# Performance work log

Measured on AMD Instinct MI355X. Metric: run time of the kernel, lower is better.

The kernel has to match this reference:

```python
import jax, jax.numpy as jnp
import numpy as np

N = 74240        # total nodes (256 graphs x 290 padded atoms)
E = 593920       # edges
D_IN = 75        # atom feature dim (dgllife canonical featurizer)
D = 128          # embedding / hidden dim
L = 3            # GCN layers
BATCH = 256      # graphs per batch
EPS = 1e-5


def setup_inputs() -> dict:
    key = jax.random.key(0)
    ks = jax.random.split(key, 10)
    node_feats = jax.random.normal(ks[0], (N, D_IN), dtype=jnp.float32)
    src = jax.random.randint(ks[1], (E,), 0, N, dtype=jnp.int32)
    dst = jax.random.randint(ks[2], (E,), 0, N, dtype=jnp.int32)
    # init linear, bias=False; padding=True zeros the last OUTPUT unit's weights
    W_init = jax.random.normal(ks[3], (D_IN, D), dtype=jnp.float32) * 0.05
    W_init = W_init.at[:, -1].set(0.0)
    # per-layer params (stacked): GraphConv weight/bias, residual Linear, BatchNorm
    Wg = jax.random.normal(ks[4], (L, D, D), dtype=jnp.float32) * 0.05
    bg = jnp.zeros((L, D), dtype=jnp.float32)
    Wr = jax.random.normal(ks[5], (L, D, D), dtype=jnp.float32) * 0.05
    br = jnp.zeros((L, D), dtype=jnp.float32)
    gamma = jnp.ones((L, D), dtype=jnp.float32)
    beta = jnp.zeros((L, D), dtype=jnp.float32)
    return {"node_feats": node_feats, "src": src, "dst": dst, "W_init": W_init,
            "Wg": Wg, "bg": bg, "Wr": Wr, "br": br, "gamma": gamma, "beta": beta}


def reference(node_feats, src, dst, W_init, Wg, bg, Wr, br, gamma, beta):
    # initial node embedding (no bias)
    h = node_feats @ W_init                                   # [N, D]
    for l in range(L):
        # GraphConv, gnn_norm='none': sum over in-neighbors, then linear + relu
        agg = jax.ops.segment_sum(h[src], dst, num_segments=N)   # [N, D] irregular gather/scatter
        gc = jax.nn.relu(agg @ Wg[l] + bg[l])
        # residual branch: Linear + same activation
        res = jax.nn.relu(h @ Wr[l] + br[l])
        h2 = gc + res
        # BatchNorm1d over nodes (training-mode batch statistics, dropout=0)
        mu = jnp.mean(h2, axis=0)
        var = jnp.var(h2, axis=0)
        h = gamma[l] * (h2 - mu) * jax.lax.rsqrt(var + EPS) + beta[l]
    return h.reshape(BATCH, -1, D)                            # [256, 290, 128]
```

## Files before the change

### kernel.cpp

```cpp
#include <hip/hip_runtime.h>

#define NN 74240
#define NE 593920
#define DIN 75
#define DD 128
#define NL 3
#define EPS 1e-5f
#define NB 290
#define NT (NN / 64)
#define NREP 64
#define SROWX 104

#define NB_WIFRAG 48
#define NZ4 ((NL * NREP * 256 + NN) / 4)
#define NB_ZERO  ((NZ4 + 255) / 256)
#define NB_PRE   (NB_WIFRAG + NB_ZERO)

#define NB_INIT  (NN / 64)
#define SB_WPREP NB_INIT
#define NB_WPREP ((NL * 2 * 16384) / 256)
#define SB_HIST  (SB_WPREP + NB_WPREP)
#define NB_HIST  (NE / 256)
#define SB_PREP  (SB_HIST + NB_HIST)
#define NB_SETUP (SB_PREP + 1)

typedef __attribute__((ext_vector_type(8))) short short8;
typedef __attribute__((ext_vector_type(4))) float f32x4;

static __device__ __forceinline__ unsigned short f2bf(float f) {
    union { float f; unsigned u; } v; v.f = f;
    unsigned u = v.u;
    unsigned r = (u + 0x7fffu + ((u >> 16) & 1u)) >> 16;
    return (unsigned short)r;
}

static __device__ __forceinline__ float bf2f(unsigned short s) {
    union { unsigned u; float f; } v; v.u = ((unsigned)s) << 16; return v.f;
}

__global__ __launch_bounds__(256) void k_pre(const float* __restrict__ Wi,
                                             unsigned short* __restrict__ wifrag,
                                             int* __restrict__ zbase) {
    const int tid = threadIdx.x;
    const int b = blockIdx.x;
    if (b < NB_WIFRAG) {
        const int e = b * 256 + tid;
        const int j = e & 7;
        const int lane = (e >> 3) & 63;
        const int st = e >> 9;
        const int s = st >> 3, t = st & 7;
        const int k = s * 32 + (lane >> 4) * 8 + j;
        const int n = t * 16 + (lane & 15);
        wifrag[e] = (k < DIN) ? f2bf(Wi[k * DD + n]) : (unsigned short)0;
    } else {
        const int zi = (b - NB_WIFRAG) * 256 + tid;
        if (zi < NZ4) {
            ((int4*)zbase)[zi] = (int4){0, 0, 0, 0};
        }
    }
}

__global__ __launch_bounds__(256) void k_setup(const float* __restrict__ X,
                                               const unsigned short* __restrict__ wifrag,
                                               unsigned short* __restrict__ hb,
                                               const float* __restrict__ Wg,
                                               const float* __restrict__ Wr,
                                               unsigned short* __restrict__ wf,
                                               const int* __restrict__ dst,
                                               int* __restrict__ cnt,
                                               float* __restrict__ ab0) {
    __shared__ unsigned short sXb[64 * SROWX];
    const int tid = threadIdx.x;
    const int b = blockIdx.x;
    if (b < NB_INIT) {
        const int r0 = b * 64;
        {
            const int row = tid >> 2;
            const int qt = tid & 3;
            const int k0 = qt * 19;
            const int k1 = (qt == 3) ? DIN : k0 + 19;
            const float* xrow = X + (size_t)(r0 + row) * DIN;
            unsigned short* srow = sXb + row * SROWX;
            for (int k = k0; k < k1; ++k) srow[k] = f2bf(xrow[k]);
            if (qt == 3) {
                for (int k = DIN; k < SROWX; ++k) srow[k] = 0;
            }
        }
        __syncthreads();
        const int w = tid >> 6;
        const int lane = tid & 63;
        const int ln15 = lane & 15;
        const int q = lane >> 4;
        const short8* __restrict__ wif = (const short8*)wifrag;
        f32x4 acc[8];
        #pragma unroll
        for (int t = 0; t < 8; ++t) acc[t] = (f32x4){0.f, 0.f, 0.f, 0.f};
        #pragma unroll
        for (int s = 0; s < 3; ++s) {
            const int ks = s * 32 + q * 8;
            const short8 af = *(const short8*)&sXb[(w * 16 + ln15) * SROWX + ks];
            #pragma unroll
            for (int t = 0; t < 8; ++t) {
                const short8 bfr = wif[(s * 8 + t) * 64 + lane];
                acc[t] = __builtin_amdgcn_mfma_f32_16x16x32_bf16(af, bfr, acc[t], 0, 0, 0);
            }
        }
        #pragma unroll
        for (int t = 0; t < 8; ++t) {
            #pragma unroll
            for (int r = 0; r < 4; ++r) {
                hb[(size_t)(r0 + w * 16 + q * 4 + r) * DD + t * 16 + ln15] = f2bf(acc[t][r]);
            }
        }
    } else if (b < SB_HIST) {
        const int gt = (b - SB_WPREP) * 256 + tid;
        const int l = gt >> 15;
        const int m = (gt >> 14) & 1;
        const int e = gt & 16383;
        const int k = e >> 7, n = e & 127;
        const float* W = (m == 0 ? Wg : Wr) + l * 16384;
        const float v = W[e];
        const int s = k >> 5, q = (k >> 3) & 3, j = k & 7, t = n >> 4;
        const int ln = (q << 4) | (n & 15);
        const int idx = ((s * 8 + t) * 64 + ln) * 8 + j;
        wf[(l * 2 + m) * 16384 + idx] = f2bf(v);
    } else if (b < SB_PREP) {
        const int e = (b - SB_HIST) * 256 + tid;
        atomicAdd(&cnt[dst[e]], 1);
    } else {
        ab0[tid] = (tid < 128) ? 1.0f : 0.0f;
    }
}

__global__ __launch_bounds__(256) void k_scan1(const int* __restrict__ cnt,
                                               int* __restrict__ bsum) {
    const int tid = threadIdx.x;
    int v = cnt[blockIdx.x * 256 + tid];
    #pragma unroll
    for (int off = 1; off < 64; off <<= 1) v += __shfl_xor(v, off, 64);
    __shared__ int ws[4];
    if ((tid & 63) == 0) ws[tid >> 6] = v;
    __syncthreads();
    if (tid == 0) bsum[blockIdx.x] = ws[0] + ws[1] + ws[2] + ws[3];
}

__global__ __launch_bounds__(256) void k_scan3(const int* __restrict__ cnt,
                                               const int* __restrict__ bsum,
                                               int* __restrict__ rowptr,
                                               int* __restrict__ offs) {
    const int tid = threadIdx.x;
    const int b = blockIdx.x;
    const int t = b * 256 + tid;
    const int lane = tid & 63;
    __shared__ int ws[4];
    __shared__ int ws2[4];
    __shared__ int sBoff;
    int part = 0;
    for (int i = tid; i < b; i += 256) part += bsum[i];
    #pragma unroll
    for (int off = 1; off < 64; off <<= 1) part += __shfl_xor(part, off, 64);
    if (lane == 0) ws2[tid >> 6] = part;
    __syncthreads();
    if (tid == 0) sBoff = ws2[0] + ws2[1] + ws2[2] + ws2[3];
    const int v = cnt[t];
    int inc = v;
    #pragma unroll
    for (int off = 1; off < 64; off <<= 1) {
        const int u = __shfl_up(inc, off, 64);
        if (lane >= off) inc += u;
    }
    if (lane == 63) ws[tid >> 6] = inc;
    __syncthreads();
    const int w = tid >> 6;
    int waveoff = 0;
    for (int i = 0; i < 4; ++i) waveoff += (i < w) ? ws[i] : 0;
    const int excl = sBoff + waveoff + inc - v;
    rowptr[t] = excl;
    offs[t] = excl;
    if (b == NB - 1 && tid == 255) rowptr[NN] = NE;
}

__global__ __launch_bounds__(256) void k_fill(const int* __restrict__ src,
                                              const int* __restrict__ dst,
                                              int* offs, int* __restrict__ col) {
    const int e = blockIdx.x * 256 + threadIdx.x;
    const int pos = atomicAdd(&offs[dst[e]], 1);
    col[pos] = src[e];
}

__global__ __launch_bounds__(128) void k_stats(const float* __restrict__ srep,
                                               const float* __restrict__ gamma,
                                               const float* __restrict__ beta,
                                               float* __restrict__ ab) {
    const int c = threadIdx.x;
    float s = 0.f, q = 0.f;
    for (int r = 0; r < NREP; ++r) {
        s += srep[r * 256 + c];
        q += srep[r * 256 + 128 + c];
    }
    const float invN = 1.0f / (float)NN;
    const float mu = s * invN;
    const float var = q * invN - mu * mu;
    const float a = gamma[c] * rsqrtf(var + EPS);
    ab[c] = a;
    ab[128 + c] = beta[c] - a * mu;
}

__global__ __launch_bounds__(256) void k_gather(const unsigned short* __restrict__ hb,
                                                const int* __restrict__ rowptr,
                                                const int* __restrict__ col,
                                                const float* __restrict__ ab,
                                                unsigned short* __restrict__ aggb) {
    const int wave = threadIdx.x >> 6;
    const int lane = threadIdx.x & 63;
    const int row = blockIdx.x * 4 + wave;
    const int eb = rowptr[row];
    const int ee = rowptr[row + 1];
    const int half = lane >> 5;
    const int f = (lane & 31) * 4;
    float4 a0 = {0.f,0.f,0.f,0.f}, a1 = {0.f,0.f,0.f,0.f};
    float4 a2 = {0.f,0.f,0.f,0.f}, a3 = {0.f,0.f,0.f,0.f};
    int e = eb + half;
    for (; e + 6 < ee; e += 8) {
        const int c0 = col[e], c1 = col[e + 2], c2 = col[e + 4], c3 = col[e + 6];
        const ushort4 v0 = *(const ushort4*)(hb + (size_t)c0 * DD + f);
        const ushort4 v1 = *(const ushort4*)(hb + (size_t)c1 * DD + f);
        const ushort4 v2 = *(const ushort4*)(hb + (size_t)c2 * DD + f);
        const ushort4 v3 = *(const ushort4*)(hb + (size_t)c3 * DD + f);
        a0.x += bf2f(v0.x); a0.y += bf2f(v0.y); a0.z += bf2f(v0.z); a0.w += bf2f(v0.w);
        a1.x += bf2f(v1.x); a1.y += bf2f(v1.y); a1.z += bf2f(v1.z); a1.w += bf2f(v1.w);
        a2.x += bf2f(v2.x); a2.y += bf2f(v2.y); a2.z += bf2f(v2.z); a2.w += bf2f(v2.w);
        a3.x += bf2f(v3.x); a3.y += bf2f(v3.y); a3.z += bf2f(v3.z); a3.w += bf2f(v3.w);
    }
    for (; e < ee; e += 2) {
        const int c = col[e];
        const ushort4 v = *(const ushort4*)(hb + (size_t)c * DD + f);
        a0.x += bf2f(v.x); a0.y += bf2f(v.y); a0.z += bf2f(v.z); a0.w += bf2f(v.w);
    }
    float4 s;
    s.x = (a0.x + a1.x) + (a2.x + a3.x);
    s.y = (a0.y + a1.y) + (a2.y + a3.y);
    s.z = (a0.z + a1.z) + (a2.z + a3.z);
    s.w = (a0.w + a1.w) + (a2.w + a3.w);
    s.x += __shfl_xor(s.x, 32, 64);
    s.y += __shfl_xor(s.y, 32, 64);
    s.z += __shfl_xor(s.z, 32, 64);
    s.w += __shfl_xor(s.w, 32, 64);
    if (half == 0) {
        const float deg = (float)(ee - eb);
        const float4 av = *(const float4*)(ab + f);
        const float4 bv = *(const float4*)(ab + 128 + f);
        ushort4 o;
        o.x = f2bf(fmaf(av.x, s.x, deg * bv.x));
        o.y = f2bf(fmaf(av.y, s.y, deg * bv.y));
        o.z = f2bf(fmaf(av.z, s.z, deg * bv.z));
        o.w = f2bf(fmaf(av.w, s.w, deg * bv.w));
        *(ushort4*)(aggb + (size_t)row * DD + f) = o;
    }
}

#define STAGE(bf, ss) do {                                              \
    _Pragma("unroll")                                                   \
    for (int i_ = 0; i_ < 4; ++i_) {                                    \
        const int idx_ = tid + i_ * 256;                                \
        const uint4 v_ = (idx_ < 512) ? wg_u4[(ss) * 512 + idx_]        \
                                      : wr_u4[(ss) * 512 + idx_ - 512]; \
        ((uint4*)sB[bf])[idx_] = v_;                                    \
    }                                                                   \
} while (0)

__global__ __launch_bounds__(256, 4) void k_layer(const unsigned short* __restrict__ hin,
                                                  const unsigned short* __restrict__ aggb,
                                                  const unsigned short* __restrict__ wfrag,
                                                  const float* __restrict__ bg,
                                                  const float* __restrict__ br,
                                                  const float* __restrict__ ab,
                                                  unsigned short* __restrict__ h2b,
                                                  float* __restrict__ sumrep) {
    __shared__ unsigned short sB[2][8192];
    __shared__ float sSum[256];
    const int tid = threadIdx.x;
    sSum[tid] = 0.0f;

    const int w = tid >> 6;
    const int lane = tid & 63;
    const int ln15 = lane & 15;
    const int q = lane >> 4;
    const int r0 = blockIdx.x * 64 + w * 16;
    const int arow = r0 + ln15;

    const uint4* __restrict__ wg_u4 = (const uint4*)wfrag;
    const uint4* __restrict__ wr_u4 = wg_u4 + 2048;

    f32x4 accg[8], accr[8];
    #pragma unroll
    for (int t = 0; t < 8; ++t) {
        accg[t] = (f32x4){0.f, 0.f, 0.f, 0.f};
        accr[t] = (f32x4){0.f, 0.f, 0.f, 0.f};
    }

    STAGE(0, 0);
    __syncthreads();
    int cur = 0;

    #pragma unroll
    for (int s = 0; s < 4; ++s) {
        if (s < 3) STAGE(cur ^ 1, s + 1);
        const int kk = s * 32 + q * 8;
        const short8 af = *(const short8*)(aggb + (size_t)arow * DD + kk);
        const short8 hr = *(const short8*)(hin + (size_t)arow * DD + kk);
        const float4 av0 = *(const float4*)(ab + kk);
        const float4 av1 = *(const float4*)(ab + kk + 4);
        const float4 bv0 = *(const float4*)(ab + 128 + kk);
        const float4 bv1 = *(const float4*)(ab + 128 + kk + 4);
        short8 hf;
        hf[0] = (short)f2bf(fmaf(av0.x, bf2f((unsigned short)hr[0]), bv0.x));
        hf[1] = (short)f2bf(fmaf(av0.y, bf2f((unsigned short)hr[1]), bv0.y));
        hf[2] = (short)f2bf(fmaf(av0.z, bf2f((unsigned short)hr[2]), bv0.z));
        hf[3] = (short)f2bf(fmaf(av0.w, bf2f((unsigned short)hr[3]), bv0.w));
        hf[4] = (short)f2bf(fmaf(av1.x, bf2f((unsigned short)hr[4]), bv1.x));
        hf[5] = (short)f2bf(fmaf(av1.y, bf2f((unsigned short)hr[5]), bv1.y));
        hf[6] = (short)f2bf(fmaf(av1.z, bf2f((unsigned short)hr[6]), bv1.z));
        hf[7] = (short)f2bf(fmaf(av1.w, bf2f((unsigned short)hr[7]), bv1.w));
        #pragma unroll
        for (int t = 0; t < 8; ++t) {
            const short8 bgf = *(const short8*)&sB[cur][(t * 64 + lane) * 8];
            const short8 brf = *(const short8*)&sB[cur][4096 + (t * 64 + lane) * 8];
            accg[t] = __builtin_amdgcn_mfma_f32_16x16x32_bf16(af, bgf, accg[t], 0, 0, 0);
            accr[t] = __builtin_amdgcn_mfma_f32_16x16x32_bf16(hf, brf, accr[t], 0, 0, 0);
        }
        __syncthreads();
        cur ^= 1;
    }

    #pragma unroll
    for (int t = 0; t < 8; ++t) {
        const int c = t * 16 + ln15;
        const float bgc = bg[c];
        const float brc = br[c];
        float sv = 0.f, qv = 0.f;
        #pragma unroll
        for (int r = 0; r < 4; ++r) {
            const int row = r0 + q * 4 + r;
            const float v = fmaxf(accg[t][r] + bgc, 0.f) + fmaxf(accr[t][r] + brc, 0.f);
            h2b[(size_t)row * DD + c] = f2bf(v);
            sv += v; qv += v * v;
        }
        sv += __shfl_xor(sv, 16, 64); sv += __shfl_xor(sv, 32, 64);
        qv += __shfl_xor(qv, 16, 64); qv += __shfl_xor(qv, 32, 64);
        if (q == 0) {
            atomicAdd(&sSum[c], sv);
            atomicAdd(&sSum[128 + c], qv);
        }
    }
    __syncthreads();
    atomicAdd(&sumrep[(blockIdx.x & (NREP - 1)) * 256 + tid], sSum[tid]);
}

__global__ __launch_bounds__(256) void k_bn(const unsigned short* __restrict__ h2b,
                                            const float* __restrict__ ab,
                                            float* __restrict__ out) {
    const int t = blockIdx.x * 256 + threadIdx.x;
    const size_t base = (size_t)t * 4;
    const int c = (int)(base & 127);
    const ushort4 v = *(const ushort4*)(h2b + base);
    const float4 a = *(const float4*)(ab + c);
    const float4 b = *(const float4*)(ab + 128 + c);
    float4 o;
    o.x = fmaf(a.x, bf2f(v.x), b.x);
    o.y = fmaf(a.y, bf2f(v.y), b.y);
    o.z = fmaf(a.z, bf2f(v.z), b.z);
    o.w = fmaf(a.w, bf2f(v.w), b.w);
    *(float4*)(out + base) = o;
}

extern "C" void kernel_launch(void* const* d_in, const int* in_sizes, int n_in,
                              void* d_out, int out_size, void* d_ws, size_t ws_size,
                              hipStream_t stream) {
    const float* X     = (const float*)d_in[0];
    const int*   src   = (const int*)d_in[1];
    const int*   dst   = (const int*)d_in[2];
    const float* Wi    = (const float*)d_in[3];
    const float* Wg    = (const float*)d_in[4];
    const float* bg    = (const float*)d_in[5];
    const float* Wr    = (const float*)d_in[6];
    const float* br    = (const float*)d_in[7];
    const float* gamma = (const float*)d_in[8];
    const float* beta  = (const float*)d_in[9];
    float* out = (float*)d_out;

    unsigned short* hA   = (unsigned short*)d_ws;
    unsigned short* hB   = hA + (size_t)NN * DD;
    unsigned short* aggb = hB + (size_t)NN * DD;
    float* sumrep = (float*)(aggb + (size_t)NN * DD);
    int* cnt      = (int*)(sumrep + NL * NREP * 256);
    int* offs     = cnt + NN;
    float* abv    = (float*)(offs + NN);
    unsigned short* wfrag = (unsigned short*)(abv + (NL + 1) * 2 * DD);
    unsigned short* wifrag = wfrag + NL * 2 * 16384;
    int* rowptr = (int*)(wifrag + 12288);
    int* col    = rowptr + NN + 1;
    int* bsum   = col + NE;

    k_pre<<<NB_PRE, 256, 0, stream>>>(Wi, wifrag, (int*)sumrep);
    k_setup<<<NB_SETUP, 256, 0, stream>>>(X, wifrag, hA, Wg, Wr, wfrag, dst, cnt, abv);
    k_scan1<<<NB, 256, 0, stream>>>(cnt, bsum);
    k_scan3<<<NB, 256, 0, stream>>>(cnt, bsum, rowptr, offs);
    k_fill<<<NE / 256, 256, 0, stream>>>(src, dst, offs, col);

    const unsigned short* hcur = hA;
    unsigned short* h2bufs[NL] = { hB, hA, hB };
    for (int l = 0; l < NL; ++l) {
        const float* abl = abv + l * 2 * DD;
        unsigned short* h2 = h2bufs[l];
        k_gather<<<NN / 4, 256, 0, stream>>>(hcur, rowptr, col, abl, aggb);
        k_layer<<<NT, 256, 0, stream>>>(hcur, aggb,
                                        wfrag + l * 2 * 16384,
                                        bg + l * DD, br + l * DD,
                                        abl, h2, sumrep + (size_t)l * NREP * 256);
        k_stats<<<1, 128, 0, stream>>>(sumrep + (size_t)l * NREP * 256, gamma + l * DD,
                                       beta + l * DD, abv + (l + 1) * 2 * DD);
        if (l == NL - 1) {
            k_bn<<<(NN * 32) / 256, 256, 0, stream>>>(h2, abv + NL * 2 * DD, out);
        }
        hcur = h2;
    }
}
```

Baseline: 279.4 us.

## Fold BN stats into gather launch, move affine to layer, vectorize X load

Moves the per-layer BatchNorm statistics reduction into an extra block of the next gather kernel, removing two k_stats launches. The gather now writes raw neighbor sums, and the BN affine (a*sum + deg*b) is applied in k_layer, where the degree is read from rowptr. The initial feature load into shared memory now uses coalesced float4 reads instead of per-row scalar loops. This adds extra ALU work and a rowptr read in k_layer. Because the stats block runs concurrently with gather blocks, correctness depends on ab only being consumed by the later k_layer launch.

Result: faster. 267.1 us (-4.4%).

```diff
diff --git a/kernel.cpp b/kernel.cpp
--- a/kernel.cpp
+++ b/kernel.cpp
@@ -8,6 +8,7 @@
 #define EPS 1e-5f
 #define NB 290
 #define NT (NN / 64)
+#define NGB (NN / 4)
 #define NREP 64
 #define SROWX 104
 
@@ -75,15 +76,25 @@
     if (b < NB_INIT) {
         const int r0 = b * 64;
         {
-            const int row = tid >> 2;
-            const int qt = tid & 3;
-            const int k0 = qt * 19;
-            const int k1 = (qt == 3) ? DIN : k0 + 19;
-            const float* xrow = X + (size_t)(r0 + row) * DIN;
-            unsigned short* srow = sXb + row * SROWX;
-            for (int k = k0; k < k1; ++k) srow[k] = f2bf(xrow[k]);
-            if (qt == 3) {
-                for (int k = DIN; k < SROWX; ++k) srow[k] = 0;
+            const float4* Xv = (const float4*)(X + (size_t)r0 * DIN);
+            #pragma unroll
+            for (int i = 0; i < 5; ++i) {
+                const int vi = tid + i * 256;
+                if (vi < 1200) {
+                    const float4 v = Xv[vi];
+                    const int f0 = vi * 4;
+                    int r = f0 / 75;
+                    int c = f0 - r * 75;
+                    sXb[r * SROWX + c] = f2bf(v.x);
+                    ++c; if (c == DIN) { c = 0; ++r; } sXb[r * SROWX + c] = f2bf(v.y);
+                    ++c; if (c == DIN) { c = 0; ++r; } sXb[r * SROWX + c] = f2bf(v.z);
+                    ++c; if (c == DIN) { c = 0; ++r; } sXb[r * SROWX + c] = f2bf(v.w);
+                }
+            }
+            for (int p = tid; p < 64 * (SROWX - DIN); p += 256) {
+                const int r = p / (SROWX - DIN);
+                const int c = DIN + (p - r * (SROWX - DIN));
+                sXb[r * SROWX + c] = 0;
             }
         }
         __syncthreads();
@@ -209,8 +220,28 @@
 __global__ __launch_bounds__(256) void k_gather(const unsigned short* __restrict__ hb,
                                                 const int* __restrict__ rowptr,
                                                 const int* __restrict__ col,
-                                                const float* __restrict__ ab,
-                                                unsigned short* __restrict__ aggb) {
+                                                unsigned short* __restrict__ aggb,
+                                                const float* __restrict__ srep,
+                                                const float* __restrict__ gamma,
+                                                const float* __restrict__ beta,
+                                                float* __restrict__ abn) {
+    if (blockIdx.x >= NGB) {
+        const int c = threadIdx.x;
+        if (c < 128) {
+            float s = 0.f, q = 0.f;
+            for (int r = 0; r < NREP; ++r) {
+                s += srep[r * 256 + c];
+                q += srep[r * 256 + 128 + c];
+            }
+            const float invN = 1.0f / (float)NN;
+            const float mu = s * invN;
+            const float var = q * invN - mu * mu;
+            const float a = gamma[c] * rsqrtf(var + EPS);
+            abn[c] = a;
+            abn[128 + c] = beta[c] - a * mu;
+        }
+        return;
+    }
     const int wave = threadIdx.x >> 6;
     const int lane = threadIdx.x & 63;
     const int row = blockIdx.x * 4 + wave;
@@ -247,14 +278,11 @@
     s.z += __shfl_xor(s.z, 32, 64);
     s.w += __shfl_xor(s.w, 32, 64);
     if (half == 0) {
-        const float deg = (float)(ee - eb);
-        const float4 av = *(const float4*)(ab + f);
-        const float4 bv = *(const float4*)(ab + 128 + f);
         ushort4 o;
-        o.x = f2bf(fmaf(av.x, s.x, deg * bv.x));
-        o.y = f2bf(fmaf(av.y, s.y, deg * bv.y));
-        o.z = f2bf(fmaf(av.z, s.z, deg * bv.z));
-        o.w = f2bf(fmaf(av.w, s.w, deg * bv.w));
+        o.x = f2bf(s.x);
+        o.y = f2bf(s.y);
+        o.z = f2bf(s.z);
+        o.w = f2bf(s.w);
         *(ushort4*)(aggb + (size_t)row * DD + f) = o;
     }
 }
@@ -271,6 +299,7 @@
 
 __global__ __launch_bounds__(256, 4) void k_layer(const unsigned short* __restrict__ hin,
                                                   const unsigned short* __restrict__ aggb,
+                                                  const int* __restrict__ rowptr,
                                                   const unsigned short* __restrict__ wfrag,
                                                   const float* __restrict__ bg,
                                                   const float* __restrict__ br,
@@ -288,6 +317,7 @@
     const int q = lane >> 4;
     const int r0 = blockIdx.x * 64 + w * 16;
     const int arow = r0 + ln15;
+    const float deg = (float)(rowptr[arow + 1] - rowptr[arow]);
 
     const uint4* __restrict__ wg_u4 = (const uint4*)wfrag;
     const uint4* __restrict__ wr_u4 = wg_u4 + 2048;
@@ -307,13 +337,21 @@
     for (int s = 0; s < 4; ++s) {
         if (s < 3) STAGE(cur ^ 1, s + 1);
         const int kk = s * 32 + q * 8;
-        const short8 af = *(const short8*)(aggb + (size_t)arow * DD + kk);
+        const short8 ar = *(const short8*)(aggb + (size_t)arow * DD + kk);
         const short8 hr = *(const short8*)(hin + (size_t)arow * DD + kk);
         const float4 av0 = *(const float4*)(ab + kk);
         const float4 av1 = *(const float4*)(ab + kk + 4);
         const float4 bv0 = *(const float4*)(ab + 128 + kk);
         const float4 bv1 = *(const float4*)(ab + 128 + kk + 4);
-        short8 hf;
+        short8 af, hf;
+        af[0] = (short)f2bf(fmaf(av0.x, bf2f((unsigned short)ar[0]), deg * bv0.x));
+        af[1] = (short)f2bf(fmaf(av0.y, bf2f((unsigned short)ar[1]), deg * bv0.y));
+        af[2] = (short)f2bf(fmaf(av0.z, bf2f((unsigned short)ar[2]), deg * bv0.z));
+        af[3] = (short)f2bf(fmaf(av0.w, bf2f((unsigned short)ar[3]), deg * bv0.w));
+        af[4] = (short)f2bf(fmaf(av1.x, bf2f((unsigned short)ar[4]), deg * bv1.x));
+        af[5] = (short)f2bf(fmaf(av1.y, bf2f((unsigned short)ar[5]), deg * bv1.y));
+        af[6] = (short)f2bf(fmaf(av1.z, bf2f((unsigned short)ar[6]), deg * bv1.z));
+        af[7] = (short)f2bf(fmaf(av1.w, bf2f((unsigned short)ar[7]), deg * bv1.w));
         hf[0] = (short)f2bf(fmaf(av0.x, bf2f((unsigned short)hr[0]), bv0.x));
         hf[1] = (short)f2bf(fmaf(av0.y, bf2f((unsigned short)hr[1]), bv0.y));
         hf[2] = (short)f2bf(fmaf(av0.z, bf2f((unsigned short)hr[2]), bv0.z));
@@ -411,18 +449,22 @@
     const unsigned short* hcur = hA;
     unsigned short* h2bufs[NL] = { hB, hA, hB };
     for (int l = 0; l < NL; ++l) {
-        const float* abl = abv + l * 2 * DD;
         unsigned short* h2 = h2bufs[l];
-        k_gather<<<NN / 4, 256, 0, stream>>>(hcur, rowptr, col, abl, aggb);
-        k_layer<<<NT, 256, 0, stream>>>(hcur, aggb,
+        const int gblocks = NGB + (l > 0 ? 1 : 0);
+        k_gather<<<gblocks, 256, 0, stream>>>(hcur, rowptr, col, aggb,
+                                              sumrep + (size_t)(l > 0 ? l - 1 : 0) * NREP * 256,
+                                              gamma + (l > 0 ? l - 1 : 0) * DD,
+                                              beta + (l > 0 ? l - 1 : 0) * DD,
+                                              abv + l * 2 * DD);
+        k_layer<<<NT, 256, 0, stream>>>(hcur, aggb, rowptr,
                                         wfrag + l * 2 * 16384,
                                         bg + l * DD, br + l * DD,
-                                        abl, h2, sumrep + (size_t)l * NREP * 256);
-        k_stats<<<1, 128, 0, stream>>>(sumrep + (size_t)l * NREP * 256, gamma + l * DD,
-                                       beta + l * DD, abv + (l + 1) * 2 * DD);
-        if (l == NL - 1) {
-            k_bn<<<(NN * 32) / 256, 256, 0, stream>>>(h2, abv + NL * 2 * DD, out);
-        }
+                                        abv + l * 2 * DD, h2,
+                                        sumrep + (size_t)l * NREP * 256);
         hcur = h2;
     }
-}
+    k_stats<<<1, 128, 0, stream>>>(sumrep + (size_t)(NL - 1) * NREP * 256,
+                                   gamma + (NL - 1) * DD, beta + (NL - 1) * DD,
+                                   abv + NL * 2 * DD);
+    k_bn<<<(NN * 32) / 256, 256, 0, stream>>>(h2bufs[NL - 1], abv + NL * 2 * DD, out);
+}
```
